# Performance work log

Hardware: AMD Instinct MI355X
Metric: run time of the kernel (lower is better)

## Reference

```python
import jax, jax.numpy as jnp
import numpy as np

VOCAB = 512
EMB = 256
HID = 64
T_HORIZON = 0.05


def setup_inputs() -> dict:
    key = jax.random.key(0)
    ks = jax.random.split(key, 6)
    B, L = 32, 4096
    x = jax.random.randint(ks[0], (B, L), 0, VOCAB, dtype=jnp.int64 if jax.config.jax_enable_x64 else jnp.int32)
    emb_table = jax.random.normal(ks[1], (VOCAB, EMB), dtype=jnp.float32)
    W1 = jax.random.normal(ks[2], (EMB, HID), dtype=jnp.float32) * (1.0 / np.sqrt(EMB))
    b1 = jnp.zeros((HID,), dtype=jnp.float32)
    W2 = jax.random.normal(ks[3], (HID, VOCAB), dtype=jnp.float32) * (1.0 / np.sqrt(HID))
    b2 = jnp.full((VOCAB,), 0.1, dtype=jnp.float32)  # torch: bias.data.fill_(0.1)
    return {"x": x, "emb_table": emb_table, "W1": W1, "b1": b1, "W2": W2, "b2": b2, "steps": 5}


def reference(x, emb_table, W1, b1, W2, b2, steps):
    """Vectorized Gillespie-style Markov jump simulation.

    Equivalent to the torch loop: intensity is computed once per step from the
    current state, then every (b, l) position samples a candidate next state
    from softmax(intensity) with the self-transition zeroed and renormalized
    (== categorical over logits with the current state masked to -inf), and
    accepts it with prob 1 - exp(-rate * dt).
    """
    V = emb_table.shape[0]
    dt = T_HORIZON / steps
    key = jax.random.key(42)
    keys = jax.random.split(key, steps)
    vocab_ids = jnp.arange(V)

    def step(x_t, k):
        # intensity: [B, L, V]
        h = jax.nn.relu(emb_table[x_t] @ W1 + b1)
        intensity = h @ W2 + b2
        # mask self-transition (softmax * (1 - onehot) then renormalize)
        self_mask = x_t[..., None] == vocab_ids  # [B, L, V] bool
        masked_logits = jnp.where(self_mask, -jnp.inf, intensity)
        k1, k2 = jax.random.split(k)
        next_state = jax.random.categorical(k1, masked_logits)  # [B, L]
        rate = jnp.take_along_axis(intensity, next_state[..., None], axis=-1)[..., 0]
        accept_prob = 1.0 - jnp.exp(-rate * dt)
        u = jax.random.uniform(k2, x_t.shape, dtype=rate.dtype)
        x_t = jnp.where(u < accept_prob, next_state.astype(x_t.dtype), x_t)
        return x_t, None

    x_final, _ = jax.lax.scan(step, x, keys)
    return x_final
```

## Files before the change

kernel.cpp:

```cpp
#include <hip/hip_runtime.h>
#include <stdint.h>


#define VOCAB  512
#define EMB    256
#define HID    64
#define NPOS   (32 * 4096)
#define STEPS  5
#define PPW    8
#define CHUNKS (NPOS / PPW)
#define NWAVE  8192

__host__ __device__ __forceinline__ void tf2x32(uint32_t k0, uint32_t k1,
                                                uint32_t x0, uint32_t x1,
                                                uint32_t& o0, uint32_t& o1) {
  uint32_t ks2 = k0 ^ k1 ^ 0x1BD11BDAu;
  x0 += k0; x1 += k1;
#define TFR(r) { x0 += x1; x1 = (x1 << (r)) | (x1 >> (32 - (r))); x1 ^= x0; }
  TFR(13) TFR(15) TFR(26) TFR(6)
  x0 += k1;  x1 += ks2 + 1u;
  TFR(17) TFR(29) TFR(16) TFR(24)
  x0 += ks2; x1 += k0 + 2u;
  TFR(13) TFR(15) TFR(26) TFR(6)
  x0 += k0;  x1 += k1 + 3u;
  TFR(17) TFR(29) TFR(16) TFR(24)
  x0 += k1;  x1 += ks2 + 4u;
  TFR(13) TFR(15) TFR(26) TFR(6)
  x0 += ks2; x1 += k0 + 5u;
#undef TFR
  o0 = x0; o1 = x1;
}

struct Keys {
  uint32_t k1a[STEPS], k1b[STEPS];
  uint32_t k2a[STEPS], k2b[STEPS];
};

__global__ __launch_bounds__(512)
void build_table(const float* __restrict__ emb,
                 const float* __restrict__ W1,
                 const float* __restrict__ b1,
                 const float* __restrict__ W2,
                 const float* __restrict__ b2,
                 float* __restrict__ I,
                 float* __restrict__ pthr) {
  const int s   = blockIdx.x;
  const int tid = threadIdx.x;
  __shared__ double part[8][HID];
  __shared__ double hd[HID];
  __shared__ float  redmax[8];

  const int hid = tid & (HID - 1);
  const int kq  = tid >> 6;
  const float* e = emb + s * EMB;
  double acc = 0.0;
#pragma unroll
  for (int ib = 0; ib < 32; ib += 16) {
    float ev[16], wv[16];
#pragma unroll
    for (int i = 0; i < 16; ++i) {
      const int k = kq + 8 * (ib + i);
      ev[i] = e[k];
      wv[i] = W1[k * HID + hid];
    }
#pragma unroll
    for (int i = 0; i < 16; ++i)
      acc += (double)ev[i] * (double)wv[i];
  }
  part[kq][hid] = acc;
  __syncthreads();
  if (kq == 0) {
    const double a = ((part[0][hid] + part[1][hid]) + (part[2][hid] + part[3][hid]))
                   + ((part[4][hid] + part[5][hid]) + (part[6][hid] + part[7][hid]));
    const float m = (float)a + b1[hid];
    hd[hid] = (double)(m > 0.0f ? m : 0.0f);
  }
  __syncthreads();

  double acc2 = 0.0;
#pragma unroll
  for (int kb = 0; kb < HID; kb += 16) {
    float wv[16];
#pragma unroll
    for (int i = 0; i < 16; ++i)
      wv[i] = W2[(kb + i) * VOCAB + tid];
#pragma unroll
    for (int i = 0; i < 16; ++i)
      acc2 += hd[kb + i] * (double)wv[i];
  }
  const float val = (float)acc2 + b2[tid];
  I[s * VOCAB + tid] = val;

  float lmax = val;
  for (int off = 32; off > 0; off >>= 1)
    lmax = fmaxf(lmax, __shfl_xor(lmax, off, 64));
  if ((tid & 63) == 0) redmax[tid >> 6] = lmax;
  __syncthreads();
  if (tid == 0) {
    float m = redmax[0];
#pragma unroll
    for (int i = 1; i < 8; ++i) m = fmaxf(m, redmax[i]);
    const float z = (-m) * 0.01f;
    pthr[s] = 1.0f - (float)exp((double)z);
  }
}

__global__ __launch_bounds__(256)
void markov_kernel(const int* __restrict__ x_in,
                   const float* __restrict__ I,
                   const float* __restrict__ pthr,
                   int* __restrict__ x_out,
                   Keys K) {
  const int lane = threadIdx.x & 63;
  const int wid  = (blockIdx.x << 2) | (threadIdx.x >> 6);
  const int qp = lane / 5;
  const int qt = lane - qp * 5;
  const float TINYF = 1.17549435e-38f;

#pragma unroll
  for (int c = 0; c < 2; ++c) {
    const int base = (wid + (c << 13)) * PPW;

    int scur = (lane < PPW) ? x_in[base + lane] : 0;
    const float pv = (lane < PPW) ? pthr[scur] : 0.0f;

    float u40 = 0.0f;
    if (lane < PPW * STEPS) {
      uint32_t w0, w1;
      tf2x32(K.k2a[qt], K.k2b[qt], 0u, (uint32_t)(base + qp), w0, w1);
      u40 = __uint_as_float((((w0 ^ w1) >> 9) | 0x3f800000u)) - 1.0f;
    }

    const float pq = __shfl(pv, qp, 64);
    const bool cand = (lane < PPW * STEPS) && (u40 < pq);
    unsigned long long mask = __ballot(cand);

    while (mask) {
      const int q = (int)__builtin_ctzll(mask);
      mask &= mask - 1;
      const int p = q / 5;
      const int t = q - p * 5;
      const int s = __builtin_amdgcn_readfirstlane(__shfl(scur, p, 64));

      const float* row = I + s * VOCAB;
      float rv[8];
#pragma unroll
      for (int j = 0; j < 8; ++j)
        rv[j] = row[lane + (j << 6)];

      const uint32_t fbase = ((uint32_t)(base + p) << 9) + (uint32_t)lane;
      uint32_t bits[8];
#pragma unroll
      for (int j = 0; j < 8; ++j) {
        uint32_t w0, w1;
        tf2x32(K.k1a[t], K.k1b[t], 0u, fbase + ((uint32_t)j << 6), w0, w1);
        bits[j] = w0 ^ w1;
      }

      float best = -__builtin_inff();
      float rbest = 0.0f;
      int bidx = 0;
#pragma unroll
      for (int j = 0; j < 8; ++j) {
        float ufv = __uint_as_float((bits[j] >> 9) | 0x3f800000u) - 1.0f;
        if (ufv == 0.0f) ufv = TINYF;
        const float g = -logf(-logf(ufv));
        const int v = lane + (j << 6);
        if (v != s) {
          const float val = rv[j] + g;
          if (val > best) { best = val; bidx = v; rbest = rv[j]; }
        }
      }
      for (int off = 32; off > 0; off >>= 1) {
        const float ob = __shfl_xor(best, off, 64);
        const int   oi = __shfl_xor(bidx, off, 64);
        const float orv = __shfl_xor(rbest, off, 64);
        if (ob > best || (ob == best && oi < bidx)) {
          best = ob; bidx = oi; rbest = orv;
        }
      }
      bidx = __builtin_amdgcn_readfirstlane(bidx);
      const float rate = rbest;
      const float z = (-rate) * 0.01f;
      const float pacc = 1.0f - (float)exp((double)z);
      const float u = __shfl(u40, q, 64);
      if (u < pacc) {
        if (lane == p) scur = bidx;
        const unsigned long long fut =
            (((1ull << (p * 5 + 5)) - 1) & ~((1ull << (q + 1)) - 1));
        const float pnew = pthr[bidx];
        const unsigned long long nb = __ballot(u40 < pnew) & fut;
        mask = (mask & ~fut) | nb;
      }
    }
    if (lane < PPW) x_out[base + lane] = scur;
  }
}

extern "C" void kernel_launch(void* const* d_in, const int* in_sizes, int n_in,
                              void* d_out, int out_size, void* d_ws, size_t ws_size,
                              hipStream_t stream) {
  const int*   x   = (const int*)d_in[0];
  const float* emb = (const float*)d_in[1];
  const float* W1  = (const float*)d_in[2];
  const float* b1  = (const float*)d_in[3];
  const float* W2  = (const float*)d_in[4];
  const float* b2  = (const float*)d_in[5];
  float* I    = (float*)d_ws;
  float* pthr = (float*)d_ws + VOCAB * VOCAB;
  int* out = (int*)d_out;

  Keys K;
  for (int t = 0; t < STEPS; ++t) {
    uint32_t Sa, Sb;
    tf2x32(0u, 42u, 0u, (uint32_t)t, Sa, Sb);
    tf2x32(Sa, Sb, 0u, 0u, K.k1a[t], K.k1b[t]);
    tf2x32(Sa, Sb, 0u, 1u, K.k2a[t], K.k2b[t]);
  }

  build_table<<<VOCAB, 512, 0, stream>>>(emb, W1, b1, W2, b2, I, pthr);
  markov_kernel<<<NWAVE / 4, 256, 0, stream>>>(x, I, pthr, out, K);
}
```

Measured before the change: 117.6 us.

## Split into screen and compacted jump kernels with fast-log prefilter

```diff
diff --git a/kernel.cpp b/kernel.cpp
--- a/kernel.cpp
+++ b/kernel.cpp
@@ -7,9 +7,7 @@
 #define HID    64
 #define NPOS   (32 * 4096)
 #define STEPS  5
-#define PPW    8
-#define CHUNKS (NPOS / PPW)
-#define NWAVE  8192
+#define JWAVES 8192
 
 __host__ __device__ __forceinline__ void tf2x32(uint32_t k0, uint32_t k1,
                                                 uint32_t x0, uint32_t x1,
@@ -43,9 +41,13 @@
                  const float* __restrict__ W2,
                  const float* __restrict__ b2,
                  float* __restrict__ I,
-                 float* __restrict__ pthr) {
+                 float* __restrict__ P,
+                 float* __restrict__ pthr,
+                 uint32_t* __restrict__ counter) {
   const int s   = blockIdx.x;
   const int tid = threadIdx.x;
+  if (s == 0 && tid == 0) *counter = 0u;
+
   __shared__ double part[8][HID];
   __shared__ double hd[HID];
   __shared__ float  redmax[8];
@@ -90,8 +92,11 @@
   }
   const float val = (float)acc2 + b2[tid];
   I[s * VOCAB + tid] = val;
-
-  float lmax = val;
+  const float z = (-val) * 0.01f;
+  const float pv = 1.0f - (float)exp((double)z);
+  P[s * VOCAB + tid] = pv;
+
+  float lmax = pv;
   for (int off = 32; off > 0; off >>= 1)
     lmax = fmaxf(lmax, __shfl_xor(lmax, off, 64));
   if ((tid & 63) == 0) redmax[tid >> 6] = lmax;
@@ -100,47 +105,79 @@
     float m = redmax[0];
 #pragma unroll
     for (int i = 1; i < 8; ++i) m = fmaxf(m, redmax[i]);
-    const float z = (-m) * 0.01f;
-    pthr[s] = 1.0f - (float)exp((double)z);
+    pthr[s] = m;
   }
 }
 
 __global__ __launch_bounds__(256)
-void markov_kernel(const int* __restrict__ x_in,
-                   const float* __restrict__ I,
+void screen_kernel(const int* __restrict__ x_in,
                    const float* __restrict__ pthr,
                    int* __restrict__ x_out,
+                   uint32_t* __restrict__ counter,
+                   uint32_t* __restrict__ list,
                    Keys K) {
+  const int pos = blockIdx.x * 256 + threadIdx.x;
+  const int s = x_in[pos];
+  const float th = pthr[s];
+  int mask = 0;
+#pragma unroll
+  for (int t = 0; t < STEPS; ++t) {
+    uint32_t w0, w1;
+    tf2x32(K.k2a[t], K.k2b[t], 0u, (uint32_t)pos, w0, w1);
+    const float u = __uint_as_float((((w0 ^ w1) >> 9) | 0x3f800000u)) - 1.0f;
+    if (u < th) mask |= (1 << t);
+  }
+  x_out[pos] = s;
+
+  const int lane = threadIdx.x & 63, wv = threadIdx.x >> 6;
+  const unsigned long long bal = __ballot(mask != 0);
+  __shared__ uint32_t wcnt[4], wbase[4];
+  if (lane == 0) wcnt[wv] = (uint32_t)__popcll(bal);
+  __syncthreads();
+  if (threadIdx.x == 0) {
+    const uint32_t tot = wcnt[0] + wcnt[1] + wcnt[2] + wcnt[3];
+    uint32_t b = atomicAdd(counter, tot);
+    wbase[0] = b; b += wcnt[0];
+    wbase[1] = b; b += wcnt[1];
+    wbase[2] = b; b += wcnt[2];
+    wbase[3] = b;
+  }
+  __syncthreads();
+  if (mask) {
+    const uint32_t off = wbase[wv] +
+        (uint32_t)__popcll(bal & ((1ull << lane) - 1ull));
+    list[off] = (uint32_t)pos | ((uint32_t)mask << 20);
+  }
+}
+
+__global__ __launch_bounds__(128)
+void jump_kernel(const int* __restrict__ x_in,
+                 const float* __restrict__ I,
+                 const float* __restrict__ P,
+                 const float* __restrict__ pthr,
+                 int* __restrict__ x_out,
+                 const uint32_t* __restrict__ counter,
+                 const uint32_t* __restrict__ list,
+                 Keys K) {
   const int lane = threadIdx.x & 63;
-  const int wid  = (blockIdx.x << 2) | (threadIdx.x >> 6);
-  const int qp = lane / 5;
-  const int qt = lane - qp * 5;
+  const int wid  = (blockIdx.x << 1) | (threadIdx.x >> 6);
+  const int n = (int)*counter;
   const float TINYF = 1.17549435e-38f;
-
-#pragma unroll
-  for (int c = 0; c < 2; ++c) {
-    const int base = (wid + (c << 13)) * PPW;
-
-    int scur = (lane < PPW) ? x_in[base + lane] : 0;
-    const float pv = (lane < PPW) ? pthr[scur] : 0.0f;
-
-    float u40 = 0.0f;
-    if (lane < PPW * STEPS) {
-      uint32_t w0, w1;
-      tf2x32(K.k2a[qt], K.k2b[qt], 0u, (uint32_t)(base + qp), w0, w1);
-      u40 = __uint_as_float((((w0 ^ w1) >> 9) | 0x3f800000u)) - 1.0f;
-    }
-
-    const float pq = __shfl(pv, qp, 64);
-    const bool cand = (lane < PPW * STEPS) && (u40 < pq);
-    unsigned long long mask = __ballot(cand);
-
-    while (mask) {
-      const int q = (int)__builtin_ctzll(mask);
-      mask &= mask - 1;
-      const int p = q / 5;
-      const int t = q - p * 5;
-      const int s = __builtin_amdgcn_readfirstlane(__shfl(scur, p, 64));
+  const float NEGINF = -__builtin_inff();
+
+  for (int i = wid; i < n; i += JWAVES) {
+    const uint32_t e = list[i];
+    const int pos = (int)(e & 0xFFFFFu);
+    int m = (int)(e >> 20);
+    int s = __builtin_amdgcn_readfirstlane(x_in[pos]);
+
+    while (m) {
+      const int t = __builtin_ctz(m);
+      m &= m - 1;
+
+      uint32_t a0, a1;
+      tf2x32(K.k2a[t], K.k2b[t], 0u, (uint32_t)pos, a0, a1);
+      const float u = __uint_as_float((((a0 ^ a1) >> 9) | 0x3f800000u)) - 1.0f;
 
       const float* row = I + s * VOCAB;
       float rv[8];
@@ -148,7 +185,7 @@
       for (int j = 0; j < 8; ++j)
         rv[j] = row[lane + (j << 6)];
 
-      const uint32_t fbase = ((uint32_t)(base + p) << 9) + (uint32_t)lane;
+      const uint32_t fbase = ((uint32_t)pos << 9) + (uint32_t)lane;
       uint32_t bits[8];
 #pragma unroll
       for (int j = 0; j < 8; ++j) {
@@ -157,43 +194,57 @@
         bits[j] = w0 ^ w1;
       }
 
-      float best = -__builtin_inff();
-      float rbest = 0.0f;
-      int bidx = 0;
+      float valC[8];
+      float bestC = NEGINF;
 #pragma unroll
       for (int j = 0; j < 8; ++j) {
         float ufv = __uint_as_float((bits[j] >> 9) | 0x3f800000u) - 1.0f;
         if (ufv == 0.0f) ufv = TINYF;
-        const float g = -logf(-logf(ufv));
+        const float gC = -__logf(-__logf(ufv));
         const int v = lane + (j << 6);
-        if (v != s) {
+        valC[j] = (v == s) ? NEGINF : rv[j] + gC;
+        bestC = fmaxf(bestC, valC[j]);
+      }
+      for (int off = 32; off > 0; off >>= 1)
+        bestC = fmaxf(bestC, __shfl_xor(bestC, off, 64));
+      const float thresh = bestC - 0.015625f;
+
+      float best = NEGINF;
+      int bidx = 0x7FFFFFFF;
+#pragma unroll
+      for (int j = 0; j < 8; ++j) {
+        if (valC[j] >= thresh) {
+          float ufv = __uint_as_float((bits[j] >> 9) | 0x3f800000u) - 1.0f;
+          if (ufv == 0.0f) ufv = TINYF;
+          const float g = -logf(-logf(ufv));
           const float val = rv[j] + g;
-          if (val > best) { best = val; bidx = v; rbest = rv[j]; }
+          const int v = lane + (j << 6);
+          if (val > best) { best = val; bidx = v; }
         }
       }
       for (int off = 32; off > 0; off >>= 1) {
         const float ob = __shfl_xor(best, off, 64);
         const int   oi = __shfl_xor(bidx, off, 64);
-        const float orv = __shfl_xor(rbest, off, 64);
-        if (ob > best || (ob == best && oi < bidx)) {
-          best = ob; bidx = oi; rbest = orv;
+        if (ob > best || (ob == best && oi < bidx)) { best = ob; bidx = oi; }
+      }
+      bidx = __builtin_amdgcn_readfirstlane(bidx);
+
+      const float pacc = P[s * VOCAB + bidx];
+      if (u < pacc) {
+        s = bidx;
+        const float th2 = pthr[s];
+        int m2 = 0;
+        for (int t2 = t + 1; t2 < STEPS; ++t2) {
+          uint32_t w0, w1;
+          tf2x32(K.k2a[t2], K.k2b[t2], 0u, (uint32_t)pos, w0, w1);
+          const float u2 =
+              __uint_as_float((((w0 ^ w1) >> 9) | 0x3f800000u)) - 1.0f;
+          if (u2 < th2) m2 |= (1 << t2);
         }
-      }
-      bidx = __builtin_amdgcn_readfirstlane(bidx);
-      const float rate = rbest;
-      const float z = (-rate) * 0.01f;
-      const float pacc = 1.0f - (float)exp((double)z);
-      const float u = __shfl(u40, q, 64);
-      if (u < pacc) {
-        if (lane == p) scur = bidx;
-        const unsigned long long fut =
-            (((1ull << (p * 5 + 5)) - 1) & ~((1ull << (q + 1)) - 1));
-        const float pnew = pthr[bidx];
-        const unsigned long long nb = __ballot(u40 < pnew) & fut;
-        mask = (mask & ~fut) | nb;
+        m = m2;
       }
     }
-    if (lane < PPW) x_out[base + lane] = scur;
+    if (lane == 0) x_out[pos] = s;
   }
 }
 
@@ -206,8 +257,11 @@
   const float* b1  = (const float*)d_in[3];
   const float* W2  = (const float*)d_in[4];
   const float* b2  = (const float*)d_in[5];
-  float* I    = (float*)d_ws;
-  float* pthr = (float*)d_ws + VOCAB * VOCAB;
+  float*    I       = (float*)d_ws;
+  float*    P       = I + VOCAB * VOCAB;
+  float*    pthr    = P + VOCAB * VOCAB;
+  uint32_t* counter = (uint32_t*)(pthr + VOCAB);
+  uint32_t* list    = counter + 32;
   int* out = (int*)d_out;
 
   Keys K;
@@ -218,6 +272,7 @@
     tf2x32(Sa, Sb, 0u, 1u, K.k2a[t], K.k2b[t]);
   }
 
-  build_table<<<VOCAB, 512, 0, stream>>>(emb, W1, b1, W2, b2, I, pthr);
-  markov_kernel<<<NWAVE / 4, 256, 0, stream>>>(x, I, pthr, out, K);
-}
+  build_table<<<VOCAB, 512, 0, stream>>>(emb, W1, b1, W2, b2, I, P, pthr, counter);
+  screen_kernel<<<NPOS / 256, 256, 0, stream>>>(x, pthr, out, counter, list, K);
+  jump_kernel<<<JWAVES / 2, 128, 0, stream>>>(x, I, P, pthr, out, counter, list, K);
+}
```

Result: faster. 111.0 us (-5.6%).
